# Kernel optimization log

Hardware: AMD Instinct MI355X
Metric: run time of the kernel (lower is better)

Reference implementation:

```python
import jax, jax.numpy as jnp
import numpy as np

B, N, D, H = 4, 2048, 64, 8

def setup_inputs() -> dict:
    key = jax.random.key(0)
    ks = jax.random.split(key, 6)
    s = 0.05
    return {
        "x":  jax.random.normal(ks[0], (B, N, D), dtype=jnp.float32),
        "Wq": jax.random.normal(ks[1], (D, D * H), dtype=jnp.float32) * s,
        "Wk": jax.random.normal(ks[2], (D, D * H), dtype=jnp.float32) * s,
        "Wv": jax.random.normal(ks[3], (D, D * H), dtype=jnp.float32) * s,
        "Wu": jax.random.normal(ks[4], (D * H, D), dtype=jnp.float32) * s,
        "bu": jnp.zeros((D,), dtype=jnp.float32),
    }

def reference(x, Wq, Wk, Wv, Wu, bu):
    b, n, d = x.shape
    h = Wq.shape[1] // d
    # projections: each head has full width d (per the original module)
    q = (x @ Wq).reshape(b, n, h, d).transpose(0, 2, 1, 3)  # [b,h,n,d]
    k = (x @ Wk).reshape(b, n, h, d).transpose(0, 2, 1, 3)
    v = (x @ Wv).reshape(b, n, h, d).transpose(0, 2, 1, 3)
    scores = jnp.einsum('bhnd,bhmd->bhnm', q, k) / jnp.sqrt(jnp.float32(d))
    w = jax.nn.softmax(scores, axis=-1)
    y = jnp.einsum('bhnm,bhmd->bhnd', w, v)          # [b,h,n,d]
    y = y.transpose(0, 2, 1, 3).reshape(b, n, h * d)  # [b,n,h*d]
    return y @ Wu + bu
```

## Files before the change

### kernel.cpp

```cpp
#include <hip/hip_runtime.h>
#include <hip/hip_bf16.h>

#define BB 4
#define NN 2048
#define DD 64
#define HH 8
#define DHH 512

typedef __bf16 bf16_t;
typedef __bf16 bf16x8 __attribute__((ext_vector_type(8)));
typedef __bf16 bf16x4 __attribute__((ext_vector_type(4)));
typedef float f32x4 __attribute__((ext_vector_type(4)));
typedef long long i64;
typedef i64 i64x2 __attribute__((ext_vector_type(2)));
typedef _Float16 f16_t;
typedef _Float16 f16x4 __attribute__((ext_vector_type(4)));
typedef __fp16 h16x2 __attribute__((ext_vector_type(2)));

__device__ __forceinline__ void dma16(const void* g, void* l) {
    __builtin_amdgcn_global_load_lds(
        (const __attribute__((address_space(1))) unsigned int*)g,
        (__attribute__((address_space(3))) unsigned int*)l,
        16, 0, 0);
}

#define MFMA   __builtin_amdgcn_mfma_f32_16x16x32_bf16
#define MFMA8  __builtin_amdgcn_mfma_f32_16x16x32_fp8_fp8
#define MFMA16F __builtin_amdgcn_mfma_f32_16x16x16f16

#define QSCALE 0.18033688011112042f


__global__ __launch_bounds__(256) void prep(
    const float* __restrict__ Wq, const float* __restrict__ Wk,
    const float* __restrict__ Wv, const float* __restrict__ Wu,
    bf16_t* __restrict__ Wqt, bf16_t* __restrict__ Wkt,
    bf16_t* __restrict__ Wvt, bf16_t* __restrict__ Wut)
{
    const int bid = blockIdx.x, tid = threadIdx.x;
    if (bid < 12) {
        const int m = bid >> 2, slice = bid & 3;
        const float* src = (m == 0) ? Wq : (m == 1) ? Wk : Wv;
        bf16_t* dst = (m == 0) ? Wqt : (m == 1) ? Wkt : Wvt;
        const float scale = (m == 0) ? QSCALE : 1.0f;
        const int dc = slice * 128 + (tid >> 1);
        const int kbase = (tid & 1) * 32;
        #pragma unroll
        for (int k0 = 0; k0 < 4; ++k0) {
            bf16x8 p;
            #pragma unroll
            for (int j = 0; j < 8; ++j)
                p[j] = (bf16_t)(src[(size_t)(kbase + k0 * 8 + j) * 512 + dc] * scale);
            *(bf16x8*)(dst + dc * 64 + kbase + k0 * 8) = p;
        }
    } else {
        const int kq = (bid - 12) * 128;
        const int dc = tid >> 2, sub = (tid & 3) * 32;
        #pragma unroll
        for (int k0 = 0; k0 < 4; ++k0) {
            bf16x8 p;
            #pragma unroll
            for (int j = 0; j < 8; ++j)
                p[j] = (bf16_t)Wu[(size_t)(kq + sub + k0 * 8 + j) * 64 + dc];
            *(bf16x8*)(Wut + dc * 512 + kq + sub + k0 * 8) = p;
        }
    }
}

__global__ __launch_bounds__(256) void qkv_mfma(
    const float* __restrict__ x, const bf16_t* __restrict__ Wqt,
    const bf16_t* __restrict__ Wkt, const bf16_t* __restrict__ Wvt,
    char* __restrict__ q8, char* __restrict__ k8, f16_t* __restrict__ vt)
{
    const int n0   = blockIdx.x * 64;
    const int h    = blockIdx.y;
    const int tid  = threadIdx.x;
    const int w    = tid >> 6;
    const int lane = tid & 63;
    const int quad = lane >> 4;
    const int c    = lane & 15;
    const int cq   = c & 7;
    const int l8   = lane >> 3;
    const int lg   = (lane & 7) ^ l8;
    const int lo   = l8 * 128 + lg * 16;
    const int sw0  = ((quad    ) ^ cq) * 16;
    const int sw1  = ((quad + 4) ^ cq) * 16;
    const int w2048 = w * 2048;

    __shared__ __align__(16) float  xs[64 * 64];
    __shared__ __align__(16) bf16_t Wqs[64 * 64], Wks[64 * 64], Wvs[64 * 64];

    {
        const int rloc = lane >> 4;
        const int s    = lane & 15;
        #pragma unroll
        for (int j = 0; j < 4; ++j) {
            int chunk = w * 4 + j;
            int r7 = (chunk * 4 + rloc) & 7;
            const char* src = (const char*)(x + (size_t)(n0 + chunk * 4 + rloc) * 64)
                            + ((s & 8) | ((s & 7) ^ r7)) * 16;
            dma16(src, (char*)xs + chunk * 1024);
        }
    }
    const char* qg = (const char*)Wqt + (size_t)h * 8192;
    const char* kg = (const char*)Wkt + (size_t)h * 8192;
    const char* vg = (const char*)Wvt + (size_t)h * 8192;
    dma16(qg + w2048 + lo,        (char*)Wqs + w2048);
    dma16(qg + w2048 + 1024 + lo, (char*)Wqs + w2048 + 1024);
    dma16(kg + w2048 + lo,        (char*)Wks + w2048);
    dma16(kg + w2048 + 1024 + lo, (char*)Wks + w2048 + 1024);
    dma16(vg + w2048 + lo,        (char*)Wvs + w2048);
    dma16(vg + w2048 + 1024 + lo, (char*)Wvs + w2048 + 1024);
    __syncthreads();

    auto xfrag = [&](int row, int kk) -> bf16x8 {
        const char* rbase = (const char*)xs + row * 256;
        int g0 = kk * 8 + ((quad * 2    ) ^ cq);
        int g1 = kk * 8 + ((quad * 2 + 1) ^ cq);
        f32x4 a = *(const f32x4*)(rbase + g0 * 16);
        f32x4 b = *(const f32x4*)(rbase + g1 * 16);
        bf16x8 r;
        r[0] = (bf16_t)a[0]; r[1] = (bf16_t)a[1]; r[2] = (bf16_t)a[2]; r[3] = (bf16_t)a[3];
        r[4] = (bf16_t)b[0]; r[5] = (bf16_t)b[1]; r[6] = (bf16_t)b[2]; r[7] = (bf16_t)b[3];
        return r;
    };

    bf16x8 xf0 = xfrag(w * 16 + c, 0);
    bf16x8 xf1 = xfrag(w * 16 + c, 1);

    const int gr = n0 + w * 16 + c;
    const int bb = gr >> 11, nn = gr & 2047;
    char* qrow_g = q8 + (((size_t)bb * HH + h) * NN + nn) * 64;
    char* krow_g = k8 + (((size_t)bb * HH + h) * NN + nn) * 64;
    const int nsw = nn & 3;

    #pragma unroll
    for (int mb = 0; mb < 4; ++mb) {
        const char* aq = (const char*)Wqs + (mb * 16 + c) * 128;
        const char* ak = (const char*)Wks + (mb * 16 + c) * 128;
        f32x4 accq = (f32x4){0.f, 0.f, 0.f, 0.f};
        f32x4 acck = (f32x4){0.f, 0.f, 0.f, 0.f};
        accq = MFMA(*(const bf16x8*)(aq + sw0), xf0, accq, 0, 0, 0);
        accq = MFMA(*(const bf16x8*)(aq + sw1), xf1, accq, 0, 0, 0);
        acck = MFMA(*(const bf16x8*)(ak + sw0), xf0, acck, 0, 0, 0);
        acck = MFMA(*(const bf16x8*)(ak + sw1), xf1, acck, 0, 0, 0);
        int g2  = (mb * 2 + (quad >> 1)) & 3;
        int off = ((quad & 1) * 4) + ((mb >> 1) * 8) + ((g2 ^ nsw) * 16);
        int pq = __builtin_amdgcn_cvt_pk_fp8_f32(accq[0], accq[1], 0, false);
        pq     = __builtin_amdgcn_cvt_pk_fp8_f32(accq[2], accq[3], pq, true);
        int pk = __builtin_amdgcn_cvt_pk_fp8_f32(acck[0], acck[1], 0, false);
        pk     = __builtin_amdgcn_cvt_pk_fp8_f32(acck[2], acck[3], pk, true);
        *(int*)(qrow_g + off) = pq;
        *(int*)(krow_g + off) = pk;
    }

    const char* wvrow = (const char*)Wvs + (w * 16 + c) * 128;
    bf16x8 vf0 = *(const bf16x8*)(wvrow + sw0);
    bf16x8 vf1 = *(const bf16x8*)(wvrow + sw1);

    const int bb2 = n0 >> 11;
    f16_t* vtrow_g = vt + (((size_t)bb2 * HH + h) * DD + (w * 16 + c)) * NN + (n0 & 2047);

    #pragma unroll
    for (int nb = 0; nb < 4; ++nb) {
        f32x4 acc = (f32x4){0.f, 0.f, 0.f, 0.f};
        acc = MFMA(xfrag(nb * 16 + c, 0), vf0, acc, 0, 0, 0);
        acc = MFMA(xfrag(nb * 16 + c, 1), vf1, acc, 0, 0, 0);
        f16x4 p = { (f16_t)acc[0], (f16_t)acc[1], (f16_t)acc[2], (f16_t)acc[3] };
        *(f16x4*)(vtrow_g + nb * 16 + quad * 4) = p;
    }
}

__global__ __launch_bounds__(256, 4) void flash_attn(
    const char* __restrict__ q8, const char* __restrict__ k8,
    const f16_t* __restrict__ vt, bf16_t* __restrict__ y)
{
    const int h    = blockIdx.x;
    const int n0   = blockIdx.y * 64;
    const int b    = blockIdx.z;
    const int tid  = threadIdx.x;
    const int w    = tid >> 6;
    const int lane = tid & 63;
    const int quad = lane >> 4;
    const int c    = lane & 15;
    const int l8   = lane >> 3;
    const int lg   = (lane & 7) ^ l8;
    const int ksw  = (quad ^ (c & 3)) * 16;

    __shared__ __align__(16) char SM[24576];

    const size_t bh = (size_t)(b * HH + h);
    const char* qp = q8 + bh * (size_t)(NN * 64);
    const char* kp = k8 + bh * (size_t)(NN * 64);
    const char* vp = (const char*)(vt + bh * (size_t)(DD * NN));

    i64x2 qf[4];
    #pragma unroll
    for (int cb = 0; cb < 4; ++cb)
        qf[cb] = *(const i64x2*)(qp + (size_t)(n0 + cb * 16 + c) * 64 + ksw);

    const char* kdma = kp + w * 1024 + lane * 16;
    const char* vdma = vp + (size_t)(w * 16 + l8) * 4096 + lg * 16;
    const int kro = (w * 16 + c) * 64 + ksw;
    const int vro = c * 128 + (((w * 2 + (quad >> 1)) ^ (c & 7)) * 16) + (quad & 1) * 8;

    dma16(kdma,          SM + w * 1024);
    dma16(vdma,          SM + 8192 + w * 2048);
    dma16(vdma + 32768,  SM + 8192 + w * 2048 + 1024);

    float lsum[4] = {0.f, 0.f, 0.f, 0.f};
    f32x4 o[4][4];
    #pragma unroll
    for (int db = 0; db < 4; ++db)
        #pragma unroll
        for (int cb = 0; cb < 4; ++cb) o[db][cb] = (f32x4){0.f, 0.f, 0.f, 0.f};

    __syncthreads();

    dma16(kdma + 4096,          SM + 4096 + w * 1024);
    dma16(vdma + 128,           SM + 16384 + w * 2048);
    dma16(vdma + 128 + 32768,   SM + 16384 + w * 2048 + 1024);

    for (int kt = 0; kt < 32; ++kt) {
        const int buf = kt & 1;
        if (kt > 0) {
            __syncthreads();
            if (kt < 31) {
                const size_t adv = (size_t)(kt + 1);
                dma16(kdma + adv * 4096,         SM + (buf ^ 1) * 4096 + w * 1024);
                dma16(vdma + adv * 128,          SM + 8192 + (buf ^ 1) * 8192 + w * 2048);
                dma16(vdma + adv * 128 + 32768,  SM + 8192 + (buf ^ 1) * 8192 + w * 2048 + 1024);
            }
        }
        const char* kb = SM + buf * 4096;
        const char* vb = SM + 8192 + buf * 8192;

        i64x2 kf = *(const i64x2*)(kb + kro);
        f16x4 vf[4];
        #pragma unroll
        for (int db = 0; db < 4; ++db)
            vf[db] = *(const f16x4*)(vb + vro + db * 2048);

        #pragma unroll
        for (int cb = 0; cb < 4; ++cb) {
            f32x4 s = (f32x4){0.f, 0.f, 0.f, 0.f};
            s = MFMA8(kf.x, qf[cb].x, s, 0, 0, 0);
            s = MFMA8(kf.y, qf[cb].y, s, 0, 0, 0);
            float p0 = __builtin_amdgcn_exp2f(s[0]);
            float p1 = __builtin_amdgcn_exp2f(s[1]);
            float p2 = __builtin_amdgcn_exp2f(s[2]);
            float p3 = __builtin_amdgcn_exp2f(s[3]);
            lsum[cb] += (p0 + p1) + (p2 + p3);
            h16x2 ab = __builtin_amdgcn_cvt_pkrtz(p0, p1);
            h16x2 cd = __builtin_amdgcn_cvt_pkrtz(p2, p3);
            f16x4 pf = { (f16_t)ab[0], (f16_t)ab[1], (f16_t)cd[0], (f16_t)cd[1] };
            #pragma unroll
            for (int db = 0; db < 4; ++db)
                o[db][cb] = MFMA16F(vf[db], pf, o[db][cb], 0, 0, 0);
        }
    }

    __syncthreads();

    char*  Ob = SM;
    float* Lb = (float*)(SM + 16384);

    #pragma unroll
    for (int cb = 0; cb < 4; ++cb) {
        lsum[cb] += __shfl_xor(lsum[cb], 16, 64);
        lsum[cb] += __shfl_xor(lsum[cb], 32, 64);
    }
    if (quad == 0) {
        #pragma unroll
        for (int cb = 0; cb < 4; ++cb)
            Lb[(w * 4 + cb) * 16 + c] = lsum[cb];
    }

    #pragma unroll
    for (int ww = 0; ww < 4; ++ww) {
        if (w == ww) {
            #pragma unroll
            for (int db = 0; db < 4; ++db) {
                #pragma unroll
                for (int cb = 0; cb < 4; ++cb) {
                    char* p = Ob + (size_t)(((db * 4 + cb) * 4 + quad) * 16 + c) * 16;
                    f32x4 v = o[db][cb];
                    if (ww > 0) v += *(const f32x4*)p;
                    *(f32x4*)p = v;
                }
            }
        }
        __syncthreads();
    }

    {
        const int n_loc = tid & 63;
        const int dq    = tid >> 6;
        const int qcb   = n_loc >> 4;
        const int cc    = n_loc & 15;
        float l = Lb[(0 * 4 + qcb) * 16 + cc] + Lb[(1 * 4 + qcb) * 16 + cc]
                + Lb[(2 * 4 + qcb) * 16 + cc] + Lb[(3 * 4 + qcb) * 16 + cc];
        float inv = 1.0f / l;
        float vals[16];
        #pragma unroll
        for (int q2 = 0; q2 < 4; ++q2) {
            f32x4 v = *(const f32x4*)(Ob
                    + (size_t)(((dq * 4 + qcb) * 4 + q2) * 16 + cc) * 16);
            vals[q2 * 4 + 0] = v[0]; vals[q2 * 4 + 1] = v[1];
            vals[q2 * 4 + 2] = v[2]; vals[q2 * 4 + 3] = v[3];
        }
        bf16x8 o0, o1;
        #pragma unroll
        for (int j = 0; j < 8; ++j) {
            o0[j] = (bf16_t)(vals[j] * inv);
            o1[j] = (bf16_t)(vals[8 + j] * inv);
        }
        bf16_t* yrow = y + bh * (size_t)(NN * DD) + (size_t)(n0 + n_loc) * DD + dq * 16;
        *(bf16x8*)(yrow)     = o0;
        *(bf16x8*)(yrow + 8) = o1;
    }
}

__global__ __launch_bounds__(256) void out_proj(
    const bf16_t* __restrict__ y,
    const bf16_t* __restrict__ Wut,
    const float* __restrict__ bu, float* __restrict__ out)
{
    const int rt   = blockIdx.x >> 1;
    const int dh   = blockIdx.x & 1;
    const int row0 = rt * 32;
    const int b    = row0 >> 11;
    const int nn0  = row0 & 2047;
    const int tid  = threadIdx.x;
    const int w    = tid >> 6;
    const int lane = tid & 63;
    const int quad = lane >> 4;
    const int c    = lane & 15;
    const int cq   = c & 7;

    __shared__ __align__(16) bf16_t ys[32 * 512];

    {
        const int hsel = lane >> 3;
        const int g7   = lane & 7;
        #pragma unroll
        for (int rr = 0; rr < 8; ++rr) {
            int row = w * 8 + rr;
            const char* src = (const char*)y
                + (((size_t)b * HH + hsel) * NN + nn0 + row) * 128
                + ((g7 ^ (row & 7)) * 16);
            dma16(src, (char*)ys + row * 1024);
        }
    }
    __syncthreads();

    const int rows16 = (w >> 1) * 16;
    const int mb     = dh * 2 + (w & 1);
    const char* yrow = (const char*)ys + (rows16 + c) * 1024;

    f32x4 acc = (f32x4){0.f, 0.f, 0.f, 0.f};
    #pragma unroll
    for (int kk = 0; kk < 16; ++kk) {
        int g = kk * 4 + quad;
        bf16x8 bfrag = *(const bf16x8*)(yrow + (((g & ~7) | ((g & 7) ^ cq)) * 16));
        bf16x8 afrag = *(const bf16x8*)((const char*)Wut
                        + (size_t)(mb * 16 + c) * 1024 + kk * 64 + quad * 16);
        acc = MFMA(afrag, bfrag, acc, 0, 0, 0);
    }

    float4 bb = *(const float4*)(bu + mb * 16 + quad * 4);
    float4 res = { acc[0] + bb.x, acc[1] + bb.y, acc[2] + bb.z, acc[3] + bb.w };
    float* op = out + (size_t)(row0 + rows16 + c) * DD + mb * 16 + quad * 4;
    *(float4*)op = res;
}

extern "C" void kernel_launch(void* const* d_in, const int* in_sizes, int n_in,
                              void* d_out, int out_size, void* d_ws, size_t ws_size,
                              hipStream_t stream) {
    const float* x  = (const float*)d_in[0];
    const float* Wq = (const float*)d_in[1];
    const float* Wk = (const float*)d_in[2];
    const float* Wv = (const float*)d_in[3];
    const float* Wu = (const float*)d_in[4];
    const float* bu = (const float*)d_in[5];
    float* out = (float*)d_out;

    const size_t SEG8 = (size_t)BB * HH * NN * 64;
    const size_t SEG  = SEG8 * 2;
    char* ws = (char*)d_ws;
    char*   q8  = ws;
    char*   k8  = ws + SEG8;
    f16_t*  vt  = (f16_t*)(ws + 2 * SEG8);
    bf16_t* y   = (bf16_t*)(ws + 2 * SEG8 + SEG);
    bf16_t* Wqt = (bf16_t*)(ws + 2 * SEG8 + 2 * SEG);
    bf16_t* Wkt = (bf16_t*)(ws + 2 * SEG8 + 2 * SEG + (1 << 16));
    bf16_t* Wvt = (bf16_t*)(ws + 2 * SEG8 + 2 * SEG + 2 * (1 << 16));
    bf16_t* Wut = (bf16_t*)(ws + 2 * SEG8 + 2 * SEG + 3 * (1 << 16));

    prep<<<dim3(16), dim3(256), 0, stream>>>(Wq, Wk, Wv, Wu, Wqt, Wkt, Wvt, Wut);
    qkv_mfma<<<dim3(128, 8), dim3(256), 0, stream>>>(x, Wqt, Wkt, Wvt, q8, k8, vt);
    flash_attn<<<dim3(HH, NN / 64, BB), dim3(256), 0, stream>>>(q8, k8, vt, y);
    out_proj<<<dim3(512), dim3(256), 0, stream>>>(y, Wut, bu, out);
}
```

Measured before the change: 128.0 us.

## Triple-buffer per-wave K/V staging with vmcnt waits and tile V layout

The projection kernel now stores V^T in 16-column tiles so each 16-key block is contiguous, and the Q/K fp8 swizzle adds an extra XOR term. The attention loop moves from double buffering with a block-wide __syncthreads per tile to triple buffering, where each wave loads only the K/V slice it later reads itself. Explicit s_waitcnt vmcnt and sched_barrier replace the barriers. The aim is to hide global-to-LDS latency and remove barrier stalls, at the cost of more LDS per block (36 KB), which may lower occupancy.

After: 232.1 us. 1.81x slower.

```diff
diff --git a/kernel.cpp b/kernel.cpp
--- a/kernel.cpp
+++ b/kernel.cpp
@@ -132,7 +132,7 @@
     const int bb = gr >> 11, nn = gr & 2047;
     char* qrow_g = q8 + (((size_t)bb * HH + h) * NN + nn) * 64;
     char* krow_g = k8 + (((size_t)bb * HH + h) * NN + nn) * 64;
-    const int nsw = nn & 3;
+    const int nsw = (nn & 3) ^ ((nn >> 2) & 3);
 
     #pragma unroll
     for (int mb = 0; mb < 4; ++mb) {
@@ -159,7 +159,8 @@
     bf16x8 vf1 = *(const bf16x8*)(wvrow + sw1);
 
     const int bb2 = n0 >> 11;
-    f16_t* vtrow_g = vt + (((size_t)bb2 * HH + h) * DD + (w * 16 + c)) * NN + (n0 & 2047);
+    f16_t* vtb = vt + ((size_t)bb2 * HH + h) * (size_t)(DD * NN)
+               + (size_t)((n0 & 2047) >> 4) * 1024 + (w * 16 + c) * 16 + quad * 4;
 
     #pragma unroll
     for (int nb = 0; nb < 4; ++nb) {
@@ -167,7 +168,7 @@
         acc = MFMA(xfrag(nb * 16 + c, 0), vf0, acc, 0, 0, 0);
         acc = MFMA(xfrag(nb * 16 + c, 1), vf1, acc, 0, 0, 0);
         f16x4 p = { (f16_t)acc[0], (f16_t)acc[1], (f16_t)acc[2], (f16_t)acc[3] };
-        *(f16x4*)(vtrow_g + nb * 16 + quad * 4) = p;
+        *(f16x4*)(vtb + nb * 1024) = p;
     }
 }
 
@@ -183,11 +184,9 @@
     const int lane = tid & 63;
     const int quad = lane >> 4;
     const int c    = lane & 15;
-    const int l8   = lane >> 3;
-    const int lg   = (lane & 7) ^ l8;
-    const int ksw  = (quad ^ (c & 3)) * 16;
-
-    __shared__ __align__(16) char SM[24576];
+    const int ksw  = (quad ^ (c & 3) ^ ((c >> 2) & 3)) * 16;
+
+    __shared__ __align__(16) char SM[36864];
 
     const size_t bh = (size_t)(b * HH + h);
     const char* qp = q8 + bh * (size_t)(NN * 64);
@@ -200,13 +199,12 @@
         qf[cb] = *(const i64x2*)(qp + (size_t)(n0 + cb * 16 + c) * 64 + ksw);
 
     const char* kdma = kp + w * 1024 + lane * 16;
-    const char* vdma = vp + (size_t)(w * 16 + l8) * 4096 + lg * 16;
-    const int kro = (w * 16 + c) * 64 + ksw;
-    const int vro = c * 128 + (((w * 2 + (quad >> 1)) ^ (c & 7)) * 16) + (quad & 1) * 8;
-
-    dma16(kdma,          SM + w * 1024);
-    dma16(vdma,          SM + 8192 + w * 2048);
-    dma16(vdma + 32768,  SM + 8192 + w * 2048 + 1024);
+    const int vlo = (lane >> 1) * 32 + (((lane & 1) ^ ((lane >> 3) & 1)) * 16);
+    const char* vdma = vp + w * 2048 + vlo;
+
+    const int kro = w * 1024 + c * 64 + ksw;
+    const int vro = 4096 + w * 2048 + c * 32
+                  + (((quad >> 1) ^ ((c >> 2) & 1)) * 16) + (quad & 1) * 8;
 
     float lsum[4] = {0.f, 0.f, 0.f, 0.f};
     f32x4 o[4][4];
@@ -215,31 +213,25 @@
         #pragma unroll
         for (int cb = 0; cb < 4; ++cb) o[db][cb] = (f32x4){0.f, 0.f, 0.f, 0.f};
 
-    __syncthreads();
-
-    dma16(kdma + 4096,          SM + 4096 + w * 1024);
-    dma16(vdma + 128,           SM + 16384 + w * 2048);
-    dma16(vdma + 128 + 32768,   SM + 16384 + w * 2048 + 1024);
-
-    for (int kt = 0; kt < 32; ++kt) {
-        const int buf = kt & 1;
-        if (kt > 0) {
-            __syncthreads();
-            if (kt < 31) {
-                const size_t adv = (size_t)(kt + 1);
-                dma16(kdma + adv * 4096,         SM + (buf ^ 1) * 4096 + w * 1024);
-                dma16(vdma + adv * 128,          SM + 8192 + (buf ^ 1) * 8192 + w * 2048);
-                dma16(vdma + adv * 128 + 32768,  SM + 8192 + (buf ^ 1) * 8192 + w * 2048 + 1024);
-            }
-        }
-        const char* kb = SM + buf * 4096;
-        const char* vb = SM + 8192 + buf * 8192;
-
+    #define STAGE(t, buf) do {                                              \
+        char* _kb = SM + (buf) * 12288;                                     \
+        dma16(kdma + (size_t)(t) * 4096,        _kb + w * 1024);            \
+        dma16(vdma + (size_t)(t) * 8192,        _kb + 4096 + w * 2048);     \
+        dma16(vdma + (size_t)(t) * 8192 + 1024, _kb + 4096 + w * 2048 + 1024); \
+    } while (0)
+
+    #define WAITV(n) do {                                                   \
+        asm volatile("s_waitcnt vmcnt(" #n ")" ::: "memory");               \
+        __builtin_amdgcn_sched_barrier(0);                                  \
+    } while (0)
+
+    auto body = [&](int buf) {
+        const char* kb = SM + buf * 12288;
         i64x2 kf = *(const i64x2*)(kb + kro);
         f16x4 vf[4];
         #pragma unroll
         for (int db = 0; db < 4; ++db)
-            vf[db] = *(const f16x4*)(vb + vro + db * 2048);
+            vf[db] = *(const f16x4*)(kb + vro + db * 512);
 
         #pragma unroll
         for (int cb = 0; cb < 4; ++cb) {
@@ -258,7 +250,23 @@
             for (int db = 0; db < 4; ++db)
                 o[db][cb] = MFMA16F(vf[db], pf, o[db][cb], 0, 0, 0);
         }
-    }
+        __builtin_amdgcn_sched_barrier(0);
+    };
+
+    STAGE(0, 0);
+    STAGE(1, 1);
+
+    for (int j = 0; j < 10; ++j) {
+        const int kt = j * 3;
+        STAGE(kt + 2, 2); WAITV(6); body(0);
+        STAGE(kt + 3, 0); WAITV(6); body(1);
+        STAGE(kt + 4, 1); WAITV(6); body(2);
+    }
+    WAITV(3); body(0);
+    WAITV(0); body(1);
+
+    #undef STAGE
+    #undef WAITV
 
     __syncthreads();
 
```
